# Performance work log

Hardware: AMD Instinct MI355X
Metric: run time of the kernel (lower is better)

Reference implementation:

```python
import jax, jax.numpy as jnp
import numpy as np

N = 100000
E = 600000
DIM = 128
EDGE_DIM = 32

def setup_inputs() -> dict:
    key = jax.random.key(0)
    ks = jax.random.split(key, 10)
    s = 1.0 / np.sqrt(DIM)
    se = 1.0 / np.sqrt(EDGE_DIM)
    return {
        "x": jax.random.normal(ks[0], (N, DIM), dtype=jnp.float32),
        "edge_index": jax.random.randint(ks[1], (2, E), 0, N, dtype=jnp.int64),
        "edge_attr": jax.random.normal(ks[2], (E, EDGE_DIM), dtype=jnp.float32),
        "We": jax.random.uniform(ks[3], (EDGE_DIM, DIM), minval=-se, maxval=se, dtype=jnp.float32),
        "be": jnp.zeros((DIM,), dtype=jnp.float32),
        "W1": jax.random.uniform(ks[4], (DIM, DIM), minval=-s, maxval=s, dtype=jnp.float32),
        "b1": jnp.zeros((DIM,), dtype=jnp.float32),
        "W2": jax.random.uniform(ks[5], (DIM, DIM), minval=-s, maxval=s, dtype=jnp.float32),
        "b2": jnp.zeros((DIM,), dtype=jnp.float32),
        "eps": jnp.float32(0.0),
        "gamma": jnp.ones((DIM,), dtype=jnp.float32),
        "beta": jnp.zeros((DIM,), dtype=jnp.float32),
    }

def reference(x, edge_index, edge_attr, We, be, W1, b1, W2, b2, eps, gamma, beta):
    i, j = edge_index[0], edge_index[1]
    # gather source node features and add transformed edge features -> [E, dim]
    msg = x[j] + (edge_attr @ We + be)
    # scatter-sum aggregate to destination nodes -> [N, dim]
    agg = jax.ops.segment_sum(msg, i, num_segments=x.shape[0])
    h = (1.0 + eps) * x + agg
    # 2-layer MLP
    out = jax.nn.relu(h @ W1 + b1) @ W2 + b2
    # LayerNorm over last dim (dropout is identity in eval)
    mu = jnp.mean(out, axis=-1, keepdims=True)
    var = jnp.var(out, axis=-1, keepdims=True)
    out = (out - mu) * jax.lax.rsqrt(var + 1e-5) * gamma + beta
    return out
```

## Files before the change

kernel.cpp:

```cpp
#include <hip/hip_runtime.h>
#include <hip/hip_bf16.h>

#define N_NODES 100000
#define N_EDGES 600000
#define DIM 128
#define EDIM 32

typedef __attribute__((ext_vector_type(8))) short bf16x8;
typedef __attribute__((ext_vector_type(4))) float f32x4;

static __device__ __forceinline__ short f2bf(float v) {
    __hip_bfloat16 h = __float2bfloat16(v);
    return *(short*)&h;
}
static __device__ __forceinline__ float bfu2f(unsigned short u) {
    return __uint_as_float(((unsigned int)u) << 16);
}

#define AGGX_OFF  0ULL
#define AGGE_OFF  25600000ULL
#define CSR_OFF   32000000ULL
#define OFF_OFF   36800000ULL
#define DEG_OFF   37200008ULL
#define BSUM_OFF  37600016ULL
#define WEW1_OFF  37600528ULL
#define XBF_OFF   37617024ULL
#define WS_NEED_XBF (XBF_OFF + 25600000ULL)
#define SCAN_NBLK 98

__global__ __launch_bounds__(1024) void compute_wew1(
    const float* __restrict__ We, const float* __restrict__ W1,
    float* __restrict__ wew1) {
    const int idx = blockIdx.x * 1024 + threadIdx.x;
    const int k = idx >> 7, d2 = idx & 127;
    float a = 0.f;
    #pragma unroll 8
    for (int d = 0; d < DIM; ++d)
        a += We[k * DIM + d] * W1[d * DIM + d2];
    wew1[k * DIM + d2] = a;
}

typedef __attribute__((ext_vector_type(8))) short short8v;
__global__ __launch_bounds__(256) void cast_x_bf16(
    const float* __restrict__ x, unsigned short* __restrict__ xbf) {
    const int total = N_NODES * DIM / 8;
    for (int i = blockIdx.x * 256 + threadIdx.x; i < total; i += gridDim.x * 256) {
        float4 a = *(const float4*)&x[(size_t)i * 8];
        float4 b = *(const float4*)&x[(size_t)i * 8 + 4];
        short8v o;
        o[0] = f2bf(a.x); o[1] = f2bf(a.y); o[2] = f2bf(a.z); o[3] = f2bf(a.w);
        o[4] = f2bf(b.x); o[5] = f2bf(b.y); o[6] = f2bf(b.z); o[7] = f2bf(b.w);
        *(short8v*)&xbf[(size_t)i * 8] = o;
    }
}

__global__ void count_deg(const int* __restrict__ eidx, int* __restrict__ cnt) {
    int e = blockIdx.x * 256 + threadIdx.x;
    if (e < N_EDGES) atomicAdd(&cnt[eidx[e]], 1);
}

__global__ __launch_bounds__(1024) void scan_blocks(
    const int* __restrict__ cnt, int* __restrict__ off, int* __restrict__ bsum) {
    const int t = blockIdx.x * 1024 + threadIdx.x;
    const int lane = threadIdx.x & 63, wv = threadIdx.x >> 6;
    int v = (t < N_NODES) ? cnt[t] : 0;
    int s = v;
    #pragma unroll
    for (int o = 1; o < 64; o <<= 1) {
        int u = __shfl_up(s, o, 64);
        if (lane >= o) s += u;
    }
    __shared__ int wsum[16];
    if (lane == 63) wsum[wv] = s;
    __syncthreads();
    if (threadIdx.x == 0) {
        int a = 0;
        #pragma unroll
        for (int w = 0; w < 16; ++w) { int tmp = wsum[w]; wsum[w] = a; a += tmp; }
        bsum[blockIdx.x] = a;
    }
    __syncthreads();
    if (t < N_NODES) off[t] = s - v + wsum[wv];
}

__global__ __launch_bounds__(1024) void scan_add2(
    int* __restrict__ off, int* __restrict__ cursor, const int* __restrict__ bsum) {
    __shared__ int pref;
    const int b = blockIdx.x;
    if (threadIdx.x < 64) {
        int v = 0;
        if ((int)threadIdx.x < b) v = bsum[threadIdx.x];
        const int i2 = threadIdx.x + 64;
        if (i2 < b) v += bsum[i2];
        #pragma unroll
        for (int o = 32; o >= 1; o >>= 1) v += __shfl_down(v, o, 64);
        if (threadIdx.x == 0) pref = v;
    }
    __syncthreads();
    const int t = b * 1024 + threadIdx.x;
    if (t < N_NODES) {
        const int val = off[t] + pref;
        off[t] = val;
        cursor[t] = val;
    } else if (t == N_NODES) {
        off[t] = N_EDGES;
    }
}

__global__ void csr_fill(const int* __restrict__ eidx, int* __restrict__ cursor,
                         int2* __restrict__ csr) {
    int e = blockIdx.x * 256 + threadIdx.x;
    if (e < N_EDGES) {
        int i = eidx[e];
        int p = atomicAdd(&cursor[i], 1);
        csr[p] = make_int2(e, eidx[N_EDGES + e]);
    }
}

template <int BF>
__global__ __launch_bounds__(256, 4) void gine_aggregate_t(
    const void* __restrict__ xsrc,
    const float* __restrict__ eattr,
    const int* __restrict__ off,
    const int2* __restrict__ csr,
    unsigned short* __restrict__ aggX,
    unsigned short* __restrict__ aggE)
{
    const int l5 = threadIdx.x & 31;
    const int nhw = (gridDim.x * 256) >> 5;
    int n = (blockIdx.x * 256 + threadIdx.x) >> 5;

    int s = off[n], e = off[n + 1];
    while (true) {
        const int n2 = n + nhw;
        int s2 = 0, e2 = 0;
        if (n2 < N_NODES) { s2 = off[n2]; e2 = off[n2 + 1]; }

        float a0 = 0.f, a1 = 0.f, a2 = 0.f, a3 = 0.f, ae = 0.f;
        for (int t0 = s; t0 < e; t0 += 8) {
            int2 cc[8];
            #pragma unroll
            for (int k = 0; k < 8; ++k)
                cc[k] = csr[min(t0 + k, e - 1)];
            float ev[8];
            if constexpr (BF) {
                const unsigned short* xb = (const unsigned short*)xsrc;
                ushort4 xv[8];
                #pragma unroll
                for (int k = 0; k < 8; ++k) {
                    xv[k] = *(const ushort4*)&xb[(size_t)cc[k].y * DIM + l5 * 4];
                    ev[k] = eattr[(size_t)cc[k].x * EDIM + l5];
                }
                #pragma unroll
                for (int k = 0; k < 8; ++k) {
                    const float msk = (t0 + k < e) ? 1.f : 0.f;
                    a0 += msk * bfu2f(xv[k].x); a1 += msk * bfu2f(xv[k].y);
                    a2 += msk * bfu2f(xv[k].z); a3 += msk * bfu2f(xv[k].w);
                    ae += msk * ev[k];
                }
            } else {
                const float* xf = (const float*)xsrc;
                float4 xv[8];
                #pragma unroll
                for (int k = 0; k < 8; ++k) {
                    xv[k] = *(const float4*)&xf[(size_t)cc[k].y * DIM + l5 * 4];
                    ev[k] = eattr[(size_t)cc[k].x * EDIM + l5];
                }
                #pragma unroll
                for (int k = 0; k < 8; ++k) {
                    const float msk = (t0 + k < e) ? 1.f : 0.f;
                    a0 += msk * xv[k].x; a1 += msk * xv[k].y;
                    a2 += msk * xv[k].z; a3 += msk * xv[k].w;
                    ae += msk * ev[k];
                }
            }
        }
        short4 hv;
        hv.x = f2bf(a0); hv.y = f2bf(a1); hv.z = f2bf(a2); hv.w = f2bf(a3);
        *(short4*)&aggX[(size_t)n * DIM + l5 * 4] = hv;
        aggE[(size_t)n * EDIM + l5] = (unsigned short)f2bf(ae);

        if (n2 >= N_NODES) break;
        n = n2; s = s2; e = e2;
    }
}

#define HROW_STRIDE 136

__global__ __launch_bounds__(1024) void gine_mlp_fused(
    const float* __restrict__ x,
    const unsigned short* __restrict__ aggX,
    const unsigned short* __restrict__ aggE,
    const int* __restrict__ off,
    const float* __restrict__ wew1,
    const float* __restrict__ be,
    const float* __restrict__ W1,
    const float* __restrict__ b1,
    const float* __restrict__ W2,
    const float* __restrict__ b2,
    const float* __restrict__ epsp,
    const float* __restrict__ gamma,
    const float* __restrict__ beta,
    float* __restrict__ out)
{
    __shared__ short Wp[2][16384];
    __shared__ short Wep[4096];
    __shared__ short hrow[16][16 * HROW_STRIDE];

    const int tid  = threadIdx.x;
    const int wave = tid >> 6;
    const int lane = tid & 63;
    const int m    = lane & 15;
    const int g    = lane >> 4;

    for (int s = wave * 2; s < wave * 2 + 2; ++s) {
        const int dt = s >> 2, kc = s & 3;
        const int krow = kc * 32 + g * 8;
        const int col  = dt * 16 + m;
        short p1[8], p2[8];
        #pragma unroll
        for (int j = 0; j < 8; ++j) {
            p1[j] = f2bf(W1[(size_t)(krow + j) * DIM + col]);
            p2[j] = f2bf(W2[(size_t)(krow + j) * DIM + col]);
        }
        #pragma unroll
        for (int j = 0; j < 8; ++j) {
            Wp[0][(s * 64 + lane) * 8 + j] = p1[j];
            Wp[1][(s * 64 + lane) * 8 + j] = p2[j];
        }
    }
    if (wave < 8) {
        const int dt = wave;
        const int col = dt * 16 + m;
        short pw[8];
        #pragma unroll
        for (int j = 0; j < 8; ++j) pw[j] = f2bf(wew1[(size_t)(g * 8 + j) * DIM + col]);
        #pragma unroll
        for (int j = 0; j < 8; ++j) Wep[(dt * 64 + lane) * 8 + j] = pw[j];
    }

    float b1v[8], b2v[8], gv[8], btv[8];
    #pragma unroll
    for (int dt = 0; dt < 8; ++dt) {
        const int d = dt * 16 + m;
        b1v[dt] = b1[d]; b2v[dt] = b2[d]; gv[dt] = gamma[d]; btv[dt] = beta[d];
    }
    const float epv = 1.0f + epsp[0];
    __syncthreads();

    short* myrow = &hrow[wave][0];
    const int ntiles = N_NODES / 16;

    for (int tile = blockIdx.x * 16 + wave; tile < ntiles; tile += gridDim.x * 16) {
        const int nbase = tile * 16;

        bf16x8 afragE = *(const bf16x8*)&aggE[(size_t)(nbase + m) * EDIM + g * 8];

        #pragma unroll
        for (int r = 0; r < 8; ++r) {
            const int idx4 = r * 64 + lane;
            const int node = idx4 >> 5, dq = idx4 & 31;
            const size_t goff = (size_t)(nbase + node) * DIM + dq * 4;
            float4 xv = *(const float4*)&x[goff];
            ushort4 au = *(const ushort4*)&aggX[goff];
            float4 bev = ((const float4*)be)[dq];
            float dgf = (float)(off[nbase + node + 1] - off[nbase + node]);
            short4 hv;
            hv.x = f2bf(epv * xv.x + bfu2f(au.x) + dgf * bev.x);
            hv.y = f2bf(epv * xv.y + bfu2f(au.y) + dgf * bev.y);
            hv.z = f2bf(epv * xv.z + bfu2f(au.z) + dgf * bev.z);
            hv.w = f2bf(epv * xv.w + bfu2f(au.w) + dgf * bev.w);
            *(short4*)&myrow[node * HROW_STRIDE + dq * 4] = hv;
        }
        __asm__ volatile("s_waitcnt lgkmcnt(0)" ::: "memory");

        f32x4 acc[8];
        #pragma unroll
        for (int dt = 0; dt < 8; ++dt) {
            bf16x8 bfrag = *(bf16x8*)&Wep[(dt * 64 + lane) * 8];
            acc[dt] = __builtin_amdgcn_mfma_f32_16x16x32_bf16(
                afragE, bfrag, (f32x4){0.f, 0.f, 0.f, 0.f}, 0, 0, 0);
        }
        #pragma unroll
        for (int kc = 0; kc < 4; ++kc) {
            bf16x8 afrag = *(bf16x8*)&myrow[m * HROW_STRIDE + kc * 32 + g * 8];
            #pragma unroll
            for (int dt = 0; dt < 8; ++dt) {
                bf16x8 bfrag = *(bf16x8*)&Wp[0][((dt * 4 + kc) * 64 + lane) * 8];
                acc[dt] = __builtin_amdgcn_mfma_f32_16x16x32_bf16(afrag, bfrag, acc[dt], 0, 0, 0);
            }
        }
        __asm__ volatile("s_waitcnt lgkmcnt(0)" ::: "memory");

        #pragma unroll
        for (int dt = 0; dt < 8; ++dt)
            #pragma unroll
            for (int q = 0; q < 4; ++q) {
                float v = fmaxf(acc[dt][q] + b1v[dt], 0.f);
                myrow[(g * 4 + q) * HROW_STRIDE + dt * 16 + m] = f2bf(v);
            }
        __asm__ volatile("s_waitcnt lgkmcnt(0)" ::: "memory");

        #pragma unroll
        for (int dt = 0; dt < 8; ++dt) acc[dt] = (f32x4){0.f, 0.f, 0.f, 0.f};
        #pragma unroll
        for (int kc = 0; kc < 4; ++kc) {
            bf16x8 afrag = *(bf16x8*)&myrow[m * HROW_STRIDE + kc * 32 + g * 8];
            #pragma unroll
            for (int dt = 0; dt < 8; ++dt) {
                bf16x8 bfrag = *(bf16x8*)&Wp[1][((dt * 4 + kc) * 64 + lane) * 8];
                acc[dt] = __builtin_amdgcn_mfma_f32_16x16x32_bf16(afrag, bfrag, acc[dt], 0, 0, 0);
            }
        }

        float s[4] = {0, 0, 0, 0}, ss[4] = {0, 0, 0, 0};
        #pragma unroll
        for (int dt = 0; dt < 8; ++dt)
            #pragma unroll
            for (int q = 0; q < 4; ++q) {
                float o = acc[dt][q] + b2v[dt];
                acc[dt][q] = o;
                s[q] += o; ss[q] += o * o;
            }
        #pragma unroll
        for (int mask = 1; mask < 16; mask <<= 1)
            #pragma unroll
            for (int q = 0; q < 4; ++q) {
                s[q]  += __shfl_xor(s[q], mask, 64);
                ss[q] += __shfl_xor(ss[q], mask, 64);
            }
        float mu[4], inv[4];
        #pragma unroll
        for (int q = 0; q < 4; ++q) {
            mu[q] = s[q] * (1.0f / DIM);
            float var = ss[q] * (1.0f / DIM) - mu[q] * mu[q];
            inv[q] = rsqrtf(var + 1e-5f);
        }
        #pragma unroll
        for (int dt = 0; dt < 8; ++dt)
            #pragma unroll
            for (int q = 0; q < 4; ++q) {
                const int node = nbase + g * 4 + q;
                out[(size_t)node * DIM + dt * 16 + m] =
                    (acc[dt][q] - mu[q]) * inv[q] * gv[dt] + btv[dt];
            }
    }
}

extern "C" void kernel_launch(void* const* d_in, const int* in_sizes, int n_in,
                              void* d_out, int out_size, void* d_ws, size_t ws_size,
                              hipStream_t stream) {
    const float* x     = (const float*)d_in[0];
    const int*   eidx  = (const int*)d_in[1];
    const float* eattr = (const float*)d_in[2];
    const float* We    = (const float*)d_in[3];
    const float* be    = (const float*)d_in[4];
    const float* W1    = (const float*)d_in[5];
    const float* b1    = (const float*)d_in[6];
    const float* W2    = (const float*)d_in[7];
    const float* b2v   = (const float*)d_in[8];
    const float* eps   = (const float*)d_in[9];
    const float* gamma = (const float*)d_in[10];
    const float* beta  = (const float*)d_in[11];
    float* out = (float*)d_out;

    char* ws = (char*)d_ws;
    unsigned short* aggX = (unsigned short*)(ws + AGGX_OFF);
    unsigned short* aggE = (unsigned short*)(ws + AGGE_OFF);
    int2*  csr  = (int2*)(ws + CSR_OFF);
    int*   off  = (int*)(ws + OFF_OFF);
    int*   cnt  = (int*)(ws + DEG_OFF);
    int*   bsum = (int*)(ws + BSUM_OFF);
    float* wew1 = (float*)(ws + WEW1_OFF);
    unsigned short* xbf = (unsigned short*)(ws + XBF_OFF);
    const bool use_bf = (ws_size >= WS_NEED_XBF);

    hipMemsetAsync(cnt, 0, 400000, stream);
    compute_wew1<<<4, 1024, 0, stream>>>(We, W1, wew1);
    if (use_bf) cast_x_bf16<<<2048, 256, 0, stream>>>(x, xbf);
    count_deg<<<(N_EDGES + 255) / 256, 256, 0, stream>>>(eidx, cnt);
    scan_blocks<<<SCAN_NBLK, 1024, 0, stream>>>(cnt, off, bsum);
    scan_add2<<<SCAN_NBLK, 1024, 0, stream>>>(off, cnt, bsum);
    csr_fill<<<(N_EDGES + 255) / 256, 256, 0, stream>>>(eidx, cnt, csr);
    if (use_bf)
        gine_aggregate_t<1><<<2048, 256, 0, stream>>>(xbf, eattr, off, csr, aggX, aggE);
    else
        gine_aggregate_t<0><<<2048, 256, 0, stream>>>(x, eattr, off, csr, aggX, aggE);
    gine_mlp_fused<<<256, 1024, 0, stream>>>(x, aggX, aggE, off, wew1, be,
                                             W1, b1, W2, b2v, eps, gamma, beta, out);
}
```

Measured before the change: 367.1 us.

## Fold self-term and bias into aggregation, permute edge attrs to CSR order in bf16

```diff
diff --git a/kernel.cpp b/kernel.cpp
--- a/kernel.cpp
+++ b/kernel.cpp
@@ -7,6 +7,7 @@
 #define EDIM 32
 
 typedef __attribute__((ext_vector_type(8))) short bf16x8;
+typedef __attribute__((ext_vector_type(8))) short short8v;
 typedef __attribute__((ext_vector_type(4))) float f32x4;
 
 static __device__ __forceinline__ short f2bf(float v) {
@@ -17,15 +18,17 @@
     return __uint_as_float(((unsigned int)u) << 16);
 }
 
-#define AGGX_OFF  0ULL
+#define HROW_OFF  0ULL
 #define AGGE_OFF  25600000ULL
 #define CSR_OFF   32000000ULL
 #define OFF_OFF   36800000ULL
 #define DEG_OFF   37200008ULL
 #define BSUM_OFF  37600016ULL
 #define WEW1_OFF  37600528ULL
-#define XBF_OFF   37617024ULL
-#define WS_NEED_XBF (XBF_OFF + 25600000ULL)
+#define XBF_OFF   37616912ULL
+#define EPERM_OFF 63216912ULL
+#define WS_TIER1  (XBF_OFF + 25600000ULL)
+#define WS_TIER2  (EPERM_OFF + 38400000ULL)
 #define SCAN_NBLK 98
 
 __global__ __launch_bounds__(1024) void compute_wew1(
@@ -40,7 +43,6 @@
     wew1[k * DIM + d2] = a;
 }
 
-typedef __attribute__((ext_vector_type(8))) short short8v;
 __global__ __launch_bounds__(256) void cast_x_bf16(
     const float* __restrict__ x, unsigned short* __restrict__ xbf) {
     const int total = N_NODES * DIM / 8;
@@ -107,28 +109,44 @@
     }
 }
 
-__global__ void csr_fill(const int* __restrict__ eidx, int* __restrict__ cursor,
-                         int2* __restrict__ csr) {
+template <int PERME>
+__global__ void csr_fill_t(const int* __restrict__ eidx, int* __restrict__ cursor,
+                           int2* __restrict__ csr,
+                           const float* __restrict__ eattr,
+                           unsigned short* __restrict__ eperm) {
     int e = blockIdx.x * 256 + threadIdx.x;
     if (e < N_EDGES) {
         int i = eidx[e];
         int p = atomicAdd(&cursor[i], 1);
         csr[p] = make_int2(e, eidx[N_EDGES + e]);
-    }
-}
-
-template <int BF>
+        if constexpr (PERME) {
+            #pragma unroll
+            for (int c = 0; c < 8; ++c) {
+                float4 v = *(const float4*)&eattr[(size_t)e * EDIM + c * 4];
+                short4 o;
+                o.x = f2bf(v.x); o.y = f2bf(v.y); o.z = f2bf(v.z); o.w = f2bf(v.w);
+                *(short4*)&eperm[(size_t)p * EDIM + c * 4] = o;
+            }
+        }
+    }
+}
+
+template <int PERME>
 __global__ __launch_bounds__(256, 4) void gine_aggregate_t(
-    const void* __restrict__ xsrc,
-    const float* __restrict__ eattr,
+    const unsigned short* __restrict__ xbf,
+    const void* __restrict__ eat,
     const int* __restrict__ off,
     const int2* __restrict__ csr,
-    unsigned short* __restrict__ aggX,
-    unsigned short* __restrict__ aggE)
+    unsigned short* __restrict__ hrowG,
+    unsigned short* __restrict__ aggE,
+    const float* __restrict__ be,
+    const float* __restrict__ epsp)
 {
     const int l5 = threadIdx.x & 31;
     const int nhw = (gridDim.x * 256) >> 5;
     int n = (blockIdx.x * 256 + threadIdx.x) >> 5;
+    const float epv = 1.0f + epsp[0];
+    const float4 bev = ((const float4*)be)[l5];
 
     int s = off[n], e = off[n + 1];
     while (true) {
@@ -138,46 +156,38 @@
 
         float a0 = 0.f, a1 = 0.f, a2 = 0.f, a3 = 0.f, ae = 0.f;
         for (int t0 = s; t0 < e; t0 += 8) {
+            int pc[8];
             int2 cc[8];
             #pragma unroll
-            for (int k = 0; k < 8; ++k)
-                cc[k] = csr[min(t0 + k, e - 1)];
-            float ev[8];
-            if constexpr (BF) {
-                const unsigned short* xb = (const unsigned short*)xsrc;
-                ushort4 xv[8];
-                #pragma unroll
-                for (int k = 0; k < 8; ++k) {
-                    xv[k] = *(const ushort4*)&xb[(size_t)cc[k].y * DIM + l5 * 4];
-                    ev[k] = eattr[(size_t)cc[k].x * EDIM + l5];
-                }
-                #pragma unroll
-                for (int k = 0; k < 8; ++k) {
-                    const float msk = (t0 + k < e) ? 1.f : 0.f;
-                    a0 += msk * bfu2f(xv[k].x); a1 += msk * bfu2f(xv[k].y);
-                    a2 += msk * bfu2f(xv[k].z); a3 += msk * bfu2f(xv[k].w);
-                    ae += msk * ev[k];
-                }
-            } else {
-                const float* xf = (const float*)xsrc;
-                float4 xv[8];
-                #pragma unroll
-                for (int k = 0; k < 8; ++k) {
-                    xv[k] = *(const float4*)&xf[(size_t)cc[k].y * DIM + l5 * 4];
-                    ev[k] = eattr[(size_t)cc[k].x * EDIM + l5];
-                }
-                #pragma unroll
-                for (int k = 0; k < 8; ++k) {
-                    const float msk = (t0 + k < e) ? 1.f : 0.f;
-                    a0 += msk * xv[k].x; a1 += msk * xv[k].y;
-                    a2 += msk * xv[k].z; a3 += msk * xv[k].w;
-                    ae += msk * ev[k];
-                }
-            }
-        }
+            for (int k = 0; k < 8; ++k) {
+                pc[k] = min(t0 + k, e - 1);
+                cc[k] = csr[pc[k]];
+            }
+            ushort4 xv[8]; float ev[8];
+            #pragma unroll
+            for (int k = 0; k < 8; ++k) {
+                xv[k] = *(const ushort4*)&xbf[(size_t)cc[k].y * DIM + l5 * 4];
+                if constexpr (PERME)
+                    ev[k] = bfu2f(((const unsigned short*)eat)[(size_t)pc[k] * EDIM + l5]);
+                else
+                    ev[k] = ((const float*)eat)[(size_t)cc[k].x * EDIM + l5];
+            }
+            #pragma unroll
+            for (int k = 0; k < 8; ++k) {
+                const float msk = (t0 + k < e) ? 1.f : 0.f;
+                a0 += msk * bfu2f(xv[k].x); a1 += msk * bfu2f(xv[k].y);
+                a2 += msk * bfu2f(xv[k].z); a3 += msk * bfu2f(xv[k].w);
+                ae += msk * ev[k];
+            }
+        }
+        const float dgf = (float)(e - s);
+        ushort4 xn = *(const ushort4*)&xbf[(size_t)n * DIM + l5 * 4];
         short4 hv;
-        hv.x = f2bf(a0); hv.y = f2bf(a1); hv.z = f2bf(a2); hv.w = f2bf(a3);
-        *(short4*)&aggX[(size_t)n * DIM + l5 * 4] = hv;
+        hv.x = f2bf(epv * bfu2f(xn.x) + a0 + dgf * bev.x);
+        hv.y = f2bf(epv * bfu2f(xn.y) + a1 + dgf * bev.y);
+        hv.z = f2bf(epv * bfu2f(xn.z) + a2 + dgf * bev.z);
+        hv.w = f2bf(epv * bfu2f(xn.w) + a3 + dgf * bev.w);
+        *(short4*)&hrowG[(size_t)n * DIM + l5 * 4] = hv;
         aggE[(size_t)n * EDIM + l5] = (unsigned short)f2bf(ae);
 
         if (n2 >= N_NODES) break;
@@ -188,17 +198,13 @@
 #define HROW_STRIDE 136
 
 __global__ __launch_bounds__(1024) void gine_mlp_fused(
-    const float* __restrict__ x,
-    const unsigned short* __restrict__ aggX,
+    const unsigned short* __restrict__ hrowG,
     const unsigned short* __restrict__ aggE,
-    const int* __restrict__ off,
     const float* __restrict__ wew1,
-    const float* __restrict__ be,
     const float* __restrict__ W1,
     const float* __restrict__ b1,
     const float* __restrict__ W2,
     const float* __restrict__ b2,
-    const float* __restrict__ epsp,
     const float* __restrict__ gamma,
     const float* __restrict__ beta,
     float* __restrict__ out)
@@ -245,7 +251,6 @@
         const int d = dt * 16 + m;
         b1v[dt] = b1[d]; b2v[dt] = b2[d]; gv[dt] = gamma[d]; btv[dt] = beta[d];
     }
-    const float epv = 1.0f + epsp[0];
     __syncthreads();
 
     short* myrow = &hrow[wave][0];
@@ -257,20 +262,11 @@
         bf16x8 afragE = *(const bf16x8*)&aggE[(size_t)(nbase + m) * EDIM + g * 8];
 
         #pragma unroll
-        for (int r = 0; r < 8; ++r) {
-            const int idx4 = r * 64 + lane;
-            const int node = idx4 >> 5, dq = idx4 & 31;
-            const size_t goff = (size_t)(nbase + node) * DIM + dq * 4;
-            float4 xv = *(const float4*)&x[goff];
-            ushort4 au = *(const ushort4*)&aggX[goff];
-            float4 bev = ((const float4*)be)[dq];
-            float dgf = (float)(off[nbase + node + 1] - off[nbase + node]);
-            short4 hv;
-            hv.x = f2bf(epv * xv.x + bfu2f(au.x) + dgf * bev.x);
-            hv.y = f2bf(epv * xv.y + bfu2f(au.y) + dgf * bev.y);
-            hv.z = f2bf(epv * xv.z + bfu2f(au.z) + dgf * bev.z);
-            hv.w = f2bf(epv * xv.w + bfu2f(au.w) + dgf * bev.w);
-            *(short4*)&myrow[node * HROW_STRIDE + dq * 4] = hv;
+        for (int r = 0; r < 4; ++r) {
+            const int idx8 = r * 64 + lane;
+            const int node = idx8 >> 4, dc = idx8 & 15;
+            short8v v = *(const short8v*)&hrowG[(size_t)(nbase + node) * DIM + dc * 8];
+            *(short8v*)&myrow[node * HROW_STRIDE + dc * 8] = v;
         }
         __asm__ volatile("s_waitcnt lgkmcnt(0)" ::: "memory");
 
@@ -365,27 +361,30 @@
     float* out = (float*)d_out;
 
     char* ws = (char*)d_ws;
-    unsigned short* aggX = (unsigned short*)(ws + AGGX_OFF);
-    unsigned short* aggE = (unsigned short*)(ws + AGGE_OFF);
+    unsigned short* hrowG = (unsigned short*)(ws + HROW_OFF);
+    unsigned short* aggE  = (unsigned short*)(ws + AGGE_OFF);
     int2*  csr  = (int2*)(ws + CSR_OFF);
     int*   off  = (int*)(ws + OFF_OFF);
     int*   cnt  = (int*)(ws + DEG_OFF);
     int*   bsum = (int*)(ws + BSUM_OFF);
     float* wew1 = (float*)(ws + WEW1_OFF);
-    unsigned short* xbf = (unsigned short*)(ws + XBF_OFF);
-    const bool use_bf = (ws_size >= WS_NEED_XBF);
-
-    hipMemsetAsync(cnt, 0, 400000, stream);
+    unsigned short* xbf   = (unsigned short*)(ws + XBF_OFF);
+    unsigned short* eperm = (unsigned short*)(ws + EPERM_OFF);
+    const bool use_perm = (ws_size >= WS_TIER2);
+
+    (void)hipMemsetAsync(cnt, 0, 400000, stream);
     compute_wew1<<<4, 1024, 0, stream>>>(We, W1, wew1);
-    if (use_bf) cast_x_bf16<<<2048, 256, 0, stream>>>(x, xbf);
+    cast_x_bf16<<<2048, 256, 0, stream>>>(x, xbf);
     count_deg<<<(N_EDGES + 255) / 256, 256, 0, stream>>>(eidx, cnt);
     scan_blocks<<<SCAN_NBLK, 1024, 0, stream>>>(cnt, off, bsum);
     scan_add2<<<SCAN_NBLK, 1024, 0, stream>>>(off, cnt, bsum);
-    csr_fill<<<(N_EDGES + 255) / 256, 256, 0, stream>>>(eidx, cnt, csr);
-    if (use_bf)
-        gine_aggregate_t<1><<<2048, 256, 0, stream>>>(xbf, eattr, off, csr, aggX, aggE);
-    else
-        gine_aggregate_t<0><<<2048, 256, 0, stream>>>(x, eattr, off, csr, aggX, aggE);
-    gine_mlp_fused<<<256, 1024, 0, stream>>>(x, aggX, aggE, off, wew1, be,
-                                             W1, b1, W2, b2v, eps, gamma, beta, out);
-}
+    if (use_perm) {
+        csr_fill_t<1><<<(N_EDGES + 255) / 256, 256, 0, stream>>>(eidx, cnt, csr, eattr, eperm);
+        gine_aggregate_t<1><<<2048, 256, 0, stream>>>(xbf, eperm, off, csr, hrowG, aggE, be, eps);
+    } else {
+        csr_fill_t<0><<<(N_EDGES + 255) / 256, 256, 0, stream>>>(eidx, cnt, csr, eattr, eperm);
+        gine_aggregate_t<0><<<2048, 256, 0, stream>>>(xbf, eattr, off, csr, hrowG, aggE, be, eps);
+    }
+    gine_mlp_fused<<<256, 1024, 0, stream>>>(hrowG, aggE, wew1,
+                                             W1, b1, W2, b2v, gamma, beta, out);
+}
```

After: 348.8 us. 1.05x faster.
